# Performance work log

Measured on AMD Instinct MI355X. Metric: run time of the kernel, lower is better.

The kernel has to match this reference:

```python
import jax, jax.numpy as jnp
import numpy as np

B, D, M, H, K = 2048, 512, 32768, 4, 64
HD = D // H  # head_dim = 128


def setup_inputs() -> dict:
    key = jax.random.key(0)
    ks = jax.random.split(key, 10)
    s = 1.0 / np.sqrt(D)
    return {
        "query": jax.random.normal(ks[0], (B, D), jnp.float32),
        "memory": jax.random.normal(ks[1], (M, D), jnp.float32),
        "Wq": jax.random.normal(ks[2], (D, D), jnp.float32) * s,
        "bq": jax.random.normal(ks[3], (D,), jnp.float32) * s,
        "Wk": jax.random.normal(ks[4], (D, D), jnp.float32) * s,
        "bk": jax.random.normal(ks[5], (D,), jnp.float32) * s,
        "Wv": jax.random.normal(ks[6], (D, D), jnp.float32) * s,
        "bv": jax.random.normal(ks[7], (D,), jnp.float32) * s,
        "Wo": jax.random.normal(ks[8], (D, D), jnp.float32) * s,
        "bo": jax.random.normal(ks[9], (D,), jnp.float32) * s,
        "k": K,
    }


def reference(query, memory, Wq, bq, Wk, bk, Wv, bv, Wo, bo, k):
    # Linear projections (torch nn.Linear: x @ W.T + b)
    Q = (query @ Wq.T + bq).reshape(B, H, HD)      # [B, H, hd]
    Kp = (memory @ Wk.T + bk).reshape(M, H, HD)    # [M, H, hd]
    V = (memory @ Wv.T + bv).reshape(M, H, HD)     # [M, H, hd]

    scores = jnp.einsum('bhd,mhd->bhm', Q, Kp) / jnp.sqrt(jnp.float32(HD))  # [B, H, M]

    # top-k retrieval over the memory axis
    topk_scores, topk_idx = jax.lax.top_k(scores, k)          # [B, H, k]
    weights = jax.nn.softmax(topk_scores, axis=-1)            # [B, H, k]

    # gather V per head: V_topk[b,h,n,:] = V[topk_idx[b,h,n], h, :]
    Vt = jnp.transpose(V, (1, 0, 2))                          # [H, M, hd]
    V_topk = Vt[jnp.arange(H)[None, :, None], topk_idx]       # [B, H, k, hd]

    attended = jnp.einsum('bhk,bhkd->bhd', weights, V_topk)   # [B, H, hd]
    attended = attended.reshape(B, D)
    return attended @ Wo.T + bo
```

## Files before the change

kernel.cpp:

```cpp
#include <hip/hip_runtime.h>
#include <hip/hip_bf16.h>
#include <stdint.h>

#define B_  2048
#define D_  512
#define M_  32768
#define H_  4
#define HD_ 128
#define K_  64
#define MS_ 4
#define SLICE_ (M_ / MS_)
#define CH_ 128
#define ROWS_ 32
#define T_  12

typedef __attribute__((ext_vector_type(8))) short short8;
typedef __attribute__((ext_vector_type(4))) float float4v;

__device__ __forceinline__ ushort f2bf_rne(float f) {
  union { float f; unsigned u; } c; c.f = f;
  unsigned r = (c.u + 0x7fffu + ((c.u >> 16) & 1u)) >> 16;
  return (ushort)r;
}
__device__ __forceinline__ float bf2f(ushort u) {
  union { unsigned u; float f; } c; c.u = ((unsigned)u) << 16;
  return c.f;
}
__device__ __forceinline__ uint32_t make_key(float s, int inv) {
  union { float f; unsigned u; } c; c.f = s;
  unsigned bf = (c.u + 0x7fffu + ((c.u >> 16) & 1u)) >> 16;
  unsigned s16 = (bf ^ ((bf >> 15) ? 0xFFFFu : 0x8000u)) & 0xFFFFu;
  return (s16 << 13) | (unsigned)inv;
}

__global__ __launch_bounds__(256) void gemm_nt_bias(
    const float* __restrict__ X, const float* __restrict__ W,
    const float* __restrict__ bias, float* __restrict__ C, int N) {
  __shared__ float As[16][132];
  __shared__ float Bs[16][132];
  const int t  = threadIdx.x;
  const int tx = t & 15, ty = t >> 4;
  const int rowbase = blockIdx.x * 128;
  const int colbase = blockIdx.y * 128;
  float acc[8][8];
  #pragma unroll
  for (int i = 0; i < 8; ++i)
    #pragma unroll
    for (int j = 0; j < 8; ++j) acc[i][j] = 0.f;

  float4 va[2], vw[2];
  auto gload = [&](int k0) {
    #pragma unroll
    for (int i = 0; i < 2; ++i) {
      int idx = t + i * 256;
      int r = idx >> 2, kq = idx & 3;
      va[i] = *(const float4*)&X[(size_t)(rowbase + r) * 512 + k0 + kq * 4];
      vw[i] = *(const float4*)&W[(size_t)(colbase + r) * 512 + k0 + kq * 4];
    }
  };
  auto sstore = [&]() {
    #pragma unroll
    for (int i = 0; i < 2; ++i) {
      int idx = t + i * 256;
      int r = idx >> 2, kq = idx & 3;
      As[kq*4+0][r] = va[i].x; As[kq*4+1][r] = va[i].y;
      As[kq*4+2][r] = va[i].z; As[kq*4+3][r] = va[i].w;
      Bs[kq*4+0][r] = vw[i].x; Bs[kq*4+1][r] = vw[i].y;
      Bs[kq*4+2][r] = vw[i].z; Bs[kq*4+3][r] = vw[i].w;
    }
  };

  gload(0);
  for (int k0 = 0; k0 < 512; k0 += 16) {
    sstore();
    __syncthreads();
    if (k0 + 16 < 512) gload(k0 + 16);
    #pragma unroll
    for (int k = 0; k < 16; ++k) {
      float a[8], b[8];
      *(float4*)&a[0] = *(const float4*)&As[k][ty*8];
      *(float4*)&a[4] = *(const float4*)&As[k][ty*8+4];
      *(float4*)&b[0] = *(const float4*)&Bs[k][tx*8];
      *(float4*)&b[4] = *(const float4*)&Bs[k][tx*8+4];
      #pragma unroll
      for (int i = 0; i < 8; ++i)
        #pragma unroll
        for (int j = 0; j < 8; ++j)
          acc[i][j] = fmaf(a[i], b[j], acc[i][j]);
    }
    __syncthreads();
  }
  #pragma unroll
  for (int i = 0; i < 8; ++i) {
    size_t r = (size_t)(rowbase + ty*8 + i);
    #pragma unroll
    for (int j4 = 0; j4 < 2; ++j4) {
      int c = colbase + tx*8 + j4*4;
      float4 bv = *(const float4*)&bias[c];
      float4 o;
      o.x = acc[i][j4*4+0] + bv.x;
      o.y = acc[i][j4*4+1] + bv.y;
      o.z = acc[i][j4*4+2] + bv.z;
      o.w = acc[i][j4*4+3] + bv.w;
      *(float4*)&C[r * 512 + c] = o;
    }
  }
}

__global__ __launch_bounds__(256) void split_w(
    const float* __restrict__ W, ushort* __restrict__ W1,
    ushort* __restrict__ W2) {
  const int i = (blockIdx.x * 256 + threadIdx.x) * 4;
  float4 v = *(const float4*)&W[i];
  float x[4] = {v.x, v.y, v.z, v.w};
  ushort u1[4] __attribute__((aligned(8)));
  ushort u2[4] __attribute__((aligned(8)));
  #pragma unroll
  for (int j = 0; j < 4; ++j) {
    u1[j] = f2bf_rne(x[j]);
    u2[j] = f2bf_rne(x[j] - bf2f(u1[j]));
  }
  *(ushort4*)&W1[i] = *(ushort4*)u1;
  *(ushort4*)&W2[i] = *(ushort4*)u2;
}

__global__ __launch_bounds__(256, 4) void gemm_split_nt(
    const float* __restrict__ X, const ushort* __restrict__ W1,
    const ushort* __restrict__ W2, const float* __restrict__ bias,
    float* __restrict__ C, int N) {
  const int t = threadIdx.x, w = t >> 6, lane = t & 63;
  const int l15 = lane & 15, l4 = lane >> 4;
  const int nb = blockIdx.x * 128 + w * 32;
  const int ob = blockIdx.y * 128;
  const short* w1s = (const short*)W1;
  const short* w2s = (const short*)W2;

  float4v acc[2][8];
  #pragma unroll
  for (int nt = 0; nt < 2; ++nt)
    #pragma unroll
    for (int ot = 0; ot < 8; ++ot) acc[nt][ot] = (float4v){0.f, 0.f, 0.f, 0.f};

  for (int ks = 0; ks < 16; ++ks) {
    short8 x1[2], x2[2];
    #pragma unroll
    for (int nt = 0; nt < 2; ++nt) {
      const float* xp = X + (size_t)(nb + nt * 16 + l15) * 512 + ks * 32 + l4 * 8;
      float xv[8];
      *(float4*)&xv[0] = *(const float4*)xp;
      *(float4*)&xv[4] = *(const float4*)(xp + 4);
      #pragma unroll
      for (int j = 0; j < 8; ++j) {
        ushort hi = f2bf_rne(xv[j]);
        ((ushort*)&x1[nt])[j] = hi;
        ((ushort*)&x2[nt])[j] = f2bf_rne(xv[j] - bf2f(hi));
      }
    }
    #pragma unroll
    for (int ot = 0; ot < 8; ++ot) {
      const size_t wo = (size_t)(ob + ot * 16 + l15) * 512 + ks * 32 + l4 * 8;
      short8 wf1 = *(const short8*)(w1s + wo);
      short8 wf2 = *(const short8*)(w2s + wo);
      #pragma unroll
      for (int nt = 0; nt < 2; ++nt) {
        acc[nt][ot] = __builtin_amdgcn_mfma_f32_16x16x32_bf16(wf1, x1[nt], acc[nt][ot], 0, 0, 0);
        acc[nt][ot] = __builtin_amdgcn_mfma_f32_16x16x32_bf16(wf2, x1[nt], acc[nt][ot], 0, 0, 0);
        acc[nt][ot] = __builtin_amdgcn_mfma_f32_16x16x32_bf16(wf1, x2[nt], acc[nt][ot], 0, 0, 0);
      }
    }
  }

  #pragma unroll
  for (int nt = 0; nt < 2; ++nt) {
    const size_t row = (size_t)(nb + nt * 16 + l15);
    #pragma unroll
    for (int ot = 0; ot < 8; ++ot) {
      const int col = ob + ot * 16 + l4 * 4;
      float4 bv = *(const float4*)&bias[col];
      float4 o;
      o.x = acc[nt][ot][0] + bv.x;
      o.y = acc[nt][ot][1] + bv.y;
      o.z = acc[nt][ot][2] + bv.z;
      o.w = acc[nt][ot][3] + bv.w;
      *(float4*)&C[row * 512 + col] = o;
    }
  }
}

__global__ __launch_bounds__(256) void to_bf16_heads(
    const float* __restrict__ src, ushort* __restrict__ dst, int nrows) {
  size_t i = (size_t)blockIdx.x * 256 + threadIdx.x;
  size_t total = (size_t)nrows * 64;
  if (i >= total) return;
  size_t m = i >> 6; int g = (int)(i & 63);
  int h = g >> 4, dd = (g & 15) << 3;
  const float* s = &src[m * 512 + (size_t)g * 8];
  ushort u[8] __attribute__((aligned(16)));
  #pragma unroll
  for (int k = 0; k < 8; ++k) u[k] = f2bf_rne(s[k]);
  *(uint4*)&dst[((size_t)h * nrows + m) * 128 + dd] = *(uint4*)u;
}

__global__ __launch_bounds__(256, 4) void scores_topk_ll(
    const ushort* __restrict__ Qbf, const ushort* __restrict__ Kbf,
    uint32_t* __restrict__ tkp) {
  const int t = threadIdx.x, w = t >> 6, lane = t & 63;
  const int l   = blockIdx.x;
  const int xcd = l & 7;
  const int i2  = l >> 3;
  const int s   = xcd + 8 * (i2 >> 6);
  const int h   = s >> 2, z = s & 3;
  const int rowbase = (i2 & 63) * ROWS_;
  const int mbase = z * SLICE_;
  const int l15 = lane & 15, l4 = lane >> 4;

  short8 qf0[4], qf1[4];
  {
    const short* Q0 = (const short*)Qbf +
        ((size_t)h * B_ + rowbase + l15) * 128 + l4 * 8;
    const short* Q1 = (const short*)Qbf +
        ((size_t)h * B_ + rowbase + 16 + l15) * 128 + l4 * 8;
    #pragma unroll
    for (int ks = 0; ks < 4; ++ks) {
      qf0[ks] = *(const short8*)(Q0 + ks * 32);
      qf1[ks] = *(const short8*)(Q1 + ks * 32);
    }
  }

  const short* Kh = (const short*)Kbf + (size_t)h * M_ * 128;

  uint32_t kt0[T_], kt1[T_];
  #pragma unroll
  for (int j = 0; j < T_; ++j) { kt0[j] = 0u; kt1[j] = 0u; }

  auto ins = [&](uint32_t c, uint32_t* kt) {
    uint32_t prev = kt[0];
    kt[0] = (kt[0] >= c) ? kt[0] : c;
    #pragma unroll
    for (int i = 1; i < T_; ++i) {
      uint32_t cur = kt[i];
      uint32_t nv;
      asm("v_med3_u32 %0, %1, %2, %3" : "=v"(nv) : "v"(prev), "v"(cur), "v"(c));
      kt[i] = nv;
      prev = cur;
    }
  };

  for (int ch = 0; ch < SLICE_ / CH_; ++ch) {
    const int mb = mbase + ch * CH_;
    short8 buf[8];
    #pragma unroll
    for (int tt = 0; tt < 2; ++tt) {
      const short* Ka = Kh + (size_t)(mb + 32 * w + 16 * tt + l15) * 128 + l4 * 8;
      #pragma unroll
      for (int ks = 0; ks < 4; ++ks)
        buf[tt * 4 + ks] = *(const short8*)(Ka + ks * 32);
    }
    #pragma unroll
    for (int tt = 0; tt < 2; ++tt) {
      const int inv0 = 8191 - (ch * CH_ + 32 * w + 16 * tt + 4 * l4);
      float4v a0 = {0.f, 0.f, 0.f, 0.f};
      float4v a1 = {0.f, 0.f, 0.f, 0.f};
      #pragma unroll
      for (int ks = 0; ks < 4; ++ks) {
        a0 = __builtin_amdgcn_mfma_f32_16x16x32_bf16(buf[tt * 4 + ks], qf0[ks], a0, 0, 0, 0);
        a1 = __builtin_amdgcn_mfma_f32_16x16x32_bf16(buf[tt * 4 + ks], qf1[ks], a1, 0, 0, 0);
      }
      #pragma unroll
      for (int reg = 0; reg < 4; ++reg) ins(make_key(a0[reg], inv0 - reg), kt0);
      #pragma unroll
      for (int reg = 0; reg < 4; ++reg) ins(make_key(a1[reg], inv0 - reg), kt1);
    }
  }

  const int id = w * 4 + l4;
  const size_t base0 =
      ((((size_t)(rowbase + l15)) * H_ + h) * MS_ + z) * (16 * T_) + (size_t)id * T_;
  const size_t base1 =
      ((((size_t)(rowbase + 16 + l15)) * H_ + h) * MS_ + z) * (16 * T_) + (size_t)id * T_;
  #pragma unroll
  for (int j = 0; j < T_; ++j) {
    tkp[base0 + j] = kt0[j];
    tkp[base1 + j] = kt1[j];
  }
}

__global__ __launch_bounds__(256) void topk_select(
    const uint32_t* __restrict__ tkp, int* __restrict__ tki) {
  __shared__ unsigned h1[256];
  __shared__ unsigned h2[256];
  __shared__ unsigned bstar, cstar, nabove;
  __shared__ int ocnt;
  __shared__ int outi[256];
  const int t = threadIdx.x;
  const int bh = blockIdx.x;
  const uint32_t* src = tkp + (size_t)bh * (MS_ * 16 * T_);
  uint32_t k[3];
  #pragma unroll
  for (int j = 0; j < 3; ++j) k[j] = src[j * 256 + t];
  h1[t] = 0; h2[t] = 0;
  if (t == 0) ocnt = 0;
  __syncthreads();
  #pragma unroll
  for (int j = 0; j < 3; ++j) atomicAdd(&h1[k[j] >> 24], 1u);
  __syncthreads();
  unsigned v = h1[t];
  for (int d = 1; d < 256; d <<= 1) {
    unsigned o = (t + d < 256) ? h1[t + d] : 0u;
    __syncthreads();
    v += o; h1[t] = v;
    __syncthreads();
  }
  if (h1[t] >= 64u && (t == 255 || h1[t + 1] < 64u)) {
    bstar = (unsigned)t; nabove = (t == 255) ? 0u : h1[t + 1];
  }
  __syncthreads();
  const unsigned bs = bstar, na = nabove;
  #pragma unroll
  for (int j = 0; j < 3; ++j)
    if ((k[j] >> 24) == bs) atomicAdd(&h2[(k[j] >> 16) & 0xFFu], 1u);
  __syncthreads();
  v = h2[t];
  for (int d = 1; d < 256; d <<= 1) {
    unsigned o = (t + d < 256) ? h2[t + d] : 0u;
    __syncthreads();
    v += o; h2[t] = v;
    __syncthreads();
  }
  if (na + h2[t] >= 64u && (t == 255 || na + h2[t + 1] < 64u)) cstar = (unsigned)t;
  __syncthreads();
  const uint32_t theta = ((((bs << 8) | cstar) << 16)) - 65536u;
  #pragma unroll
  for (int j = 0; j < 3; ++j) {
    if (k[j] >= theta) {
      int p = atomicAdd(&ocnt, 1);
      if (p < 256) {
        const int pos = j * 256 + t;
        const int z = pos / (16 * T_);
        const int ci = 8191 - (int)(k[j] & 0x1FFFu);
        outi[p] = (z << 13) | ci;
      }
    }
  }
  __syncthreads();
  int n = ocnt; if (n > 256) n = 256;
  if (t >= n) outi[t] = -(t + 1);
  __syncthreads();
  tki[(size_t)bh * 256 + t] = outi[t];
}

__global__ __launch_bounds__(256) void rescore_attend(
    const float* __restrict__ Qp, const float* __restrict__ Kp,
    const float* __restrict__ Vp, const int* __restrict__ tki,
    float* __restrict__ att) {
  __shared__ float q_[128];
  __shared__ float s_[256];
  __shared__ int   i_[256];
  __shared__ float wsm[64];
  __shared__ int   widx[64];
  const int bh = blockIdx.x, b = bh >> 2, h = bh & 3;
  const int t = threadIdx.x, w = t >> 6, lane = t & 63;
  const float SCALE = 0.08838834764831843f;

  if (t < 32) *(float4*)&q_[t * 4] = *(const float4*)&Qp[(size_t)b * 512 + h * 128 + t * 4];
  i_[t] = tki[(size_t)bh * 256 + t];
  __syncthreads();

  const int o = lane >> 3, il = lane & 7;
  #pragma unroll 2
  for (int p = 0; p < 8; ++p) {
    const int j = w * 64 + p * 8 + o;
    const int idx = i_[j];
    const float* kr = Kp + (size_t)(idx < 0 ? 0 : idx) * 512 + h * 128;
    float part = 0.f;
    #pragma unroll
    for (int u = 0; u < 4; ++u) {
      const int f = il + u * 8;
      float4 kv = *(const float4*)&kr[f * 4];
      float4 qv = *(const float4*)&q_[f * 4];
      part += kv.x * qv.x + kv.y * qv.y + kv.z * qv.z + kv.w * qv.w;
    }
    part += __shfl_xor(part, 1);
    part += __shfl_xor(part, 2);
    part += __shfl_xor(part, 4);
    if (il == 0) s_[j] = (idx < 0) ? -3.0e38f : part * SCALE;
  }
  __syncthreads();

  for (int k = 2; k <= 256; k <<= 1) {
    for (int j = k >> 1; j > 0; j >>= 1) {
      if (t < 128) {
        const int i = ((t & ~(j - 1)) << 1) | (t & (j - 1));
        const int p2 = i | j;
        const bool dir = ((i & k) == 0);
        float sa = s_[i], sb = s_[p2];
        int   ia = i_[i], ib = i_[p2];
        const bool inorder = (sa > sb) || (sa == sb && ia <= ib);
        if (inorder != dir) { s_[i] = sb; s_[p2] = sa; i_[i] = ib; i_[p2] = ia; }
      }
      __syncthreads();
    }
  }

  if (t < 64) {
    float sv = s_[t];
    float mx = sv;
    #pragma unroll
    for (int off = 32; off; off >>= 1) mx = fmaxf(mx, __shfl_xor(mx, off));
    float e = expf(sv - mx);
    float zz = e;
    #pragma unroll
    for (int off = 32; off; off >>= 1) zz += __shfl_xor(zz, off);
    wsm[t] = e / zz;
    widx[t] = i_[t];
  }
  __syncthreads();

  if (t < 128) {
    float a = 0.f;
    #pragma unroll 4
    for (int k2 = 0; k2 < 64; ++k2)
      a = fmaf(wsm[k2], Vp[(size_t)widx[k2] * 512 + h * 128 + t], a);
    att[(size_t)b * 512 + h * 128 + t] = a;
  }
}

extern "C" void kernel_launch(void* const* d_in, const int* in_sizes, int n_in,
                              void* d_out, int out_size, void* d_ws, size_t ws_size,
                              hipStream_t stream) {
  const float* query  = (const float*)d_in[0];
  const float* memory = (const float*)d_in[1];
  const float* Wq = (const float*)d_in[2];
  const float* bq = (const float*)d_in[3];
  const float* Wk = (const float*)d_in[4];
  const float* bk = (const float*)d_in[5];
  const float* Wv = (const float*)d_in[6];
  const float* bv = (const float*)d_in[7];
  const float* Wo = (const float*)d_in[8];
  const float* bo = (const float*)d_in[9];
  float* out = (float*)d_out;

  float*  Qp  = (float*)d_ws;
  float*  Kp  = Qp + (size_t)B_ * D_;
  float*  Vp  = Kp + (size_t)M_ * D_;
  int*    tki = (int*)(Vp + (size_t)M_ * D_);
  ushort* Qbf = (ushort*)(tki + (size_t)B_ * H_ * 256);
  ushort* Kbf = Qbf + (size_t)H_ * B_ * 128;
  uint32_t* tkp = (uint32_t*)Vp;
  float*  att = (float*)Kbf;
  ushort* w1v = Kbf + (size_t)2 * 1024 * 1024;
  ushort* w2v = w1v + (size_t)D_ * D_;

  gemm_nt_bias<<<dim3(B_ / 128, 4), 256, 0, stream>>>(query,  Wq, bq, Qp, B_);
  gemm_nt_bias<<<dim3(M_ / 128, 4), 256, 0, stream>>>(memory, Wk, bk, Kp, M_);

  to_bf16_heads<<<dim3((B_ * 64 + 255) / 256), 256, 0, stream>>>(Qp, Qbf, B_);
  to_bf16_heads<<<dim3((M_ * 64 + 255) / 256), 256, 0, stream>>>(Kp, Kbf, M_);

  scores_topk_ll<<<dim3(1024), 256, 0, stream>>>(Qbf, Kbf, tkp);
  topk_select<<<dim3(B_ * H_), 256, 0, stream>>>(tkp, tki);

  split_w<<<dim3(256), 256, 0, stream>>>(Wv, w1v, w2v);
  gemm_split_nt<<<dim3(M_ / 128, 4), 256, 0, stream>>>(memory, w1v, w2v, bv, Vp, M_);

  rescore_attend<<<dim3(B_ * H_), 256, 0, stream>>>(Qp, Kp, Vp, tki, att);

  gemm_nt_bias<<<dim3(B_ / 128, 4), 256, 0, stream>>>(att, Wo, bo, out, B_);
}
```

Measured before the change: 855.7 us.

## Fuse bf16 head conversion into projection GEMM and double memory slices for top-k

The separate to_bf16_heads kernels are removed, and the Q/K projection GEMM epilogue now writes the head-major bf16 copy directly. This avoids re-reading the fp32 projections. The memory axis is also split into 8 slices instead of 4, so scores_topk_ll launches 2048 blocks for more parallelism. In exchange, topk_select now processes twice as many candidate keys per row, and the slice/index encoding changes to 12 bits. The fused epilogue writes are 8-byte strided stores, which may coalesce less well.

```diff
diff --git a/kernel.cpp b/kernel.cpp
--- a/kernel.cpp
+++ b/kernel.cpp
@@ -8,7 +8,7 @@
 #define H_  4
 #define HD_ 128
 #define K_  64
-#define MS_ 4
+#define MS_ 8
 #define SLICE_ (M_ / MS_)
 #define CH_ 128
 #define ROWS_ 32
@@ -35,7 +35,8 @@
 
 __global__ __launch_bounds__(256) void gemm_nt_bias(
     const float* __restrict__ X, const float* __restrict__ W,
-    const float* __restrict__ bias, float* __restrict__ C, int N) {
+    const float* __restrict__ bias, float* __restrict__ C, int N,
+    ushort* __restrict__ Cbf) {
   __shared__ float As[16][132];
   __shared__ float Bs[16][132];
   const int t  = threadIdx.x;
@@ -90,6 +91,7 @@
     }
     __syncthreads();
   }
+  const int hh = colbase >> 7;
   #pragma unroll
   for (int i = 0; i < 8; ++i) {
     size_t r = (size_t)(rowbase + ty*8 + i);
@@ -103,6 +105,13 @@
       o.z = acc[i][j4*4+2] + bv.z;
       o.w = acc[i][j4*4+3] + bv.w;
       *(float4*)&C[r * 512 + c] = o;
+      if (Cbf) {
+        ushort u[4] __attribute__((aligned(8)));
+        u[0] = f2bf_rne(o.x); u[1] = f2bf_rne(o.y);
+        u[2] = f2bf_rne(o.z); u[3] = f2bf_rne(o.w);
+        const int dd = tx * 8 + j4 * 4;
+        *(ushort4*)&Cbf[((size_t)hh * N + r) * 128 + dd] = *(ushort4*)u;
+      }
     }
   }
 }
@@ -187,20 +196,6 @@
   }
 }
 
-__global__ __launch_bounds__(256) void to_bf16_heads(
-    const float* __restrict__ src, ushort* __restrict__ dst, int nrows) {
-  size_t i = (size_t)blockIdx.x * 256 + threadIdx.x;
-  size_t total = (size_t)nrows * 64;
-  if (i >= total) return;
-  size_t m = i >> 6; int g = (int)(i & 63);
-  int h = g >> 4, dd = (g & 15) << 3;
-  const float* s = &src[m * 512 + (size_t)g * 8];
-  ushort u[8] __attribute__((aligned(16)));
-  #pragma unroll
-  for (int k = 0; k < 8; ++k) u[k] = f2bf_rne(s[k]);
-  *(uint4*)&dst[((size_t)h * nrows + m) * 128 + dd] = *(uint4*)u;
-}
-
 __global__ __launch_bounds__(256, 4) void scores_topk_ll(
     const ushort* __restrict__ Qbf, const ushort* __restrict__ Kbf,
     uint32_t* __restrict__ tkp) {
@@ -209,7 +204,7 @@
   const int xcd = l & 7;
   const int i2  = l >> 3;
   const int s   = xcd + 8 * (i2 >> 6);
-  const int h   = s >> 2, z = s & 3;
+  const int h   = s >> 3, z = s & 7;
   const int rowbase = (i2 & 63) * ROWS_;
   const int mbase = z * SLICE_;
   const int l15 = lane & 15, l4 = lane >> 4;
@@ -258,7 +253,7 @@
     }
     #pragma unroll
     for (int tt = 0; tt < 2; ++tt) {
-      const int inv0 = 8191 - (ch * CH_ + 32 * w + 16 * tt + 4 * l4);
+      const int inv0 = SLICE_ - 1 - (ch * CH_ + 32 * w + 16 * tt + 4 * l4);
       float4v a0 = {0.f, 0.f, 0.f, 0.f};
       float4v a1 = {0.f, 0.f, 0.f, 0.f};
       #pragma unroll
@@ -295,14 +290,14 @@
   const int t = threadIdx.x;
   const int bh = blockIdx.x;
   const uint32_t* src = tkp + (size_t)bh * (MS_ * 16 * T_);
-  uint32_t k[3];
-  #pragma unroll
-  for (int j = 0; j < 3; ++j) k[j] = src[j * 256 + t];
+  uint32_t k[6];
+  #pragma unroll
+  for (int j = 0; j < 6; ++j) k[j] = src[j * 256 + t];
   h1[t] = 0; h2[t] = 0;
   if (t == 0) ocnt = 0;
   __syncthreads();
   #pragma unroll
-  for (int j = 0; j < 3; ++j) atomicAdd(&h1[k[j] >> 24], 1u);
+  for (int j = 0; j < 6; ++j) atomicAdd(&h1[k[j] >> 24], 1u);
   __syncthreads();
   unsigned v = h1[t];
   for (int d = 1; d < 256; d <<= 1) {
@@ -317,7 +312,7 @@
   __syncthreads();
   const unsigned bs = bstar, na = nabove;
   #pragma unroll
-  for (int j = 0; j < 3; ++j)
+  for (int j = 0; j < 6; ++j)
     if ((k[j] >> 24) == bs) atomicAdd(&h2[(k[j] >> 16) & 0xFFu], 1u);
   __syncthreads();
   v = h2[t];
@@ -331,14 +326,14 @@
   __syncthreads();
   const uint32_t theta = ((((bs << 8) | cstar) << 16)) - 65536u;
   #pragma unroll
-  for (int j = 0; j < 3; ++j) {
+  for (int j = 0; j < 6; ++j) {
     if (k[j] >= theta) {
       int p = atomicAdd(&ocnt, 1);
       if (p < 256) {
         const int pos = j * 256 + t;
         const int z = pos / (16 * T_);
-        const int ci = 8191 - (int)(k[j] & 0x1FFFu);
-        outi[p] = (z << 13) | ci;
+        const int ci = (SLICE_ - 1) - (int)(k[j] & 0x1FFFu);
+        outi[p] = (z << 12) | ci;
       }
     }
   }
@@ -451,13 +446,10 @@
   ushort* w1v = Kbf + (size_t)2 * 1024 * 1024;
   ushort* w2v = w1v + (size_t)D_ * D_;
 
-  gemm_nt_bias<<<dim3(B_ / 128, 4), 256, 0, stream>>>(query,  Wq, bq, Qp, B_);
-  gemm_nt_bias<<<dim3(M_ / 128, 4), 256, 0, stream>>>(memory, Wk, bk, Kp, M_);
-
-  to_bf16_heads<<<dim3((B_ * 64 + 255) / 256), 256, 0, stream>>>(Qp, Qbf, B_);
-  to_bf16_heads<<<dim3((M_ * 64 + 255) / 256), 256, 0, stream>>>(Kp, Kbf, M_);
-
-  scores_topk_ll<<<dim3(1024), 256, 0, stream>>>(Qbf, Kbf, tkp);
+  gemm_nt_bias<<<dim3(B_ / 128, 4), 256, 0, stream>>>(query,  Wq, bq, Qp, B_, Qbf);
+  gemm_nt_bias<<<dim3(M_ / 128, 4), 256, 0, stream>>>(memory, Wk, bk, Kp, M_, Kbf);
+
+  scores_topk_ll<<<dim3(2048), 256, 0, stream>>>(Qbf, Kbf, tkp);
   topk_select<<<dim3(B_ * H_), 256, 0, stream>>>(tkp, tki);
 
   split_w<<<dim3(256), 256, 0, stream>>>(Wv, w1v, w2v);
@@ -465,5 +457,5 @@
 
   rescore_attend<<<dim3(B_ * H_), 256, 0, stream>>>(Qp, Kp, Vp, tki, att);
 
-  gemm_nt_bias<<<dim3(B_ / 128, 4), 256, 0, stream>>>(att, Wo, bo, out, B_);
-}
+  gemm_nt_bias<<<dim3(B_ / 128, 4), 256, 0, stream>>>(att, Wo, bo, out, B_, nullptr);
+}
```

Result: no change. 865.8 us (+1.2%).
